# Optimization experiments

Measured on AMD Instinct MI355X. Metric: run time of the kernel, lower is better.

The kernel has to match this reference:

```python
import jax, jax.numpy as jnp
import numpy as np

B = 4; C_IN = 4; H = 32; W = 32; L = H * W
D_MODEL = 768; DEPTH = 4; D_INNER = 1536; D_STATE = 16; DT_RANK = 48; D_CONV = 4; FREQ = 256


def _zigzag_orders():
    idx = np.arange(L).reshape(H, W)
    z = idx.copy(); z[1::2] = z[1::2, ::-1]; row = z.reshape(-1)
    zt = idx.T.copy(); zt[1::2] = zt[1::2, ::-1]; col = zt.reshape(-1)
    base = [row, row[::-1].copy(), col, col[::-1].copy()]
    return np.stack([base[i % 4] for i in range(DEPTH)]).astype(np.int32)


def _sincos_pos_embed():
    def emb1d(dim, pos):
        omega = 1.0 / 10000 ** (np.arange(dim // 2, dtype=np.float64) / (dim / 2.0))
        out = np.einsum('m,d->md', pos.reshape(-1), omega)
        return np.concatenate([np.sin(out), np.cos(out)], axis=1)
    grid = np.stack(np.meshgrid(np.arange(W, dtype=np.float32), np.arange(H, dtype=np.float32)), 0)
    emb = np.concatenate([emb1d(D_MODEL // 2, grid[0]), emb1d(D_MODEL // 2, grid[1])], axis=1)
    return jnp.asarray(emb[None].astype(np.float32))  # [1, L, D]


def setup_inputs() -> dict:
    key = jax.random.key(0)
    ks = iter(jax.random.split(key, 24))
    def nrm(shape, s=0.02):
        return jax.random.normal(next(ks), shape, jnp.float32) * s
    inp = {}
    inp['x'] = jax.random.normal(next(ks), (B, C_IN, H, W), jnp.float32)
    inp['t'] = jax.random.uniform(next(ks), (B,), jnp.float32) * 1000.0
    inp['patch_w'] = nrm((D_MODEL, C_IN))
    inp['patch_b'] = jnp.zeros((D_MODEL,), jnp.float32)
    inp['pos_embed'] = _sincos_pos_embed()
    inp['t_w1'] = nrm((D_MODEL, FREQ))
    inp['t_b1'] = jnp.zeros((D_MODEL,), jnp.float32)
    inp['t_w2'] = nrm((D_MODEL, D_MODEL))
    inp['t_b2'] = jnp.zeros((D_MODEL,), jnp.float32)
    inp['norm_w'] = jnp.ones((DEPTH, D_MODEL), jnp.float32)
    inp['norm_b'] = jnp.zeros((DEPTH, D_MODEL), jnp.float32)
    inp['in_proj_w'] = nrm((DEPTH, 2 * D_INNER, D_MODEL))
    inp['conv_w'] = nrm((DEPTH, D_INNER, 1, D_CONV), 0.1)
    inp['conv_b'] = jnp.zeros((DEPTH, D_INNER), jnp.float32)
    inp['x_proj_w'] = nrm((DEPTH, DT_RANK + 2 * D_STATE, D_INNER))
    inp['dt_w'] = nrm((DEPTH, D_INNER, DT_RANK))
    inp['dt_b'] = jnp.full((DEPTH, D_INNER), -4.6, jnp.float32)  # softplus ~ 0.01
    inp['A_log'] = jnp.tile(jnp.log(jnp.arange(1, D_STATE + 1, dtype=jnp.float32)), (DEPTH, D_INNER, 1))
    inp['Dp'] = jnp.ones((DEPTH, D_INNER), jnp.float32)
    inp['out_proj_w'] = nrm((DEPTH, D_MODEL, D_INNER))
    inp['final_ada_w'] = nrm((2 * D_MODEL, D_MODEL))
    inp['final_ada_b'] = jnp.zeros((2 * D_MODEL,), jnp.float32)
    inp['final_lin_w'] = nrm((C_IN, D_MODEL))
    inp['final_lin_b'] = jnp.zeros((C_IN,), jnp.float32)
    inp['orders'] = jnp.asarray(_zigzag_orders())
    return inp


def _ln(v, w, b, eps=1e-5):
    m = v.mean(-1, keepdims=True)
    var = v.var(-1, keepdims=True)
    return (v - m) * jax.lax.rsqrt(var + eps) * w + b


def _forward(x, t, patch_w, patch_b, pos_embed, t_w1, t_b1, t_w2, t_b2, norm_w, norm_b,
             in_proj_w, conv_w, conv_b, x_proj_w, dt_w, dt_b, A_log, Dp, out_proj_w,
             final_ada_w, final_ada_b, final_lin_w, final_lin_b, orders):
    silu = jax.nn.silu
    # patch embed (patch_size=1): [B,C,H,W] -> [B,L,D]
    tok = x.reshape(B, C_IN, L).transpose(0, 2, 1)
    h = tok @ patch_w.T + patch_b + pos_embed
    # timestep embedding -> conditioning c
    half = FREQ // 2
    freqs = jnp.exp(-jnp.log(10000.0) * jnp.arange(half, dtype=jnp.float32) / half)
    ang = t[:, None] * freqs[None]
    temb = jnp.concatenate([jnp.cos(ang), jnp.sin(ang)], -1)
    c = silu(temb @ t_w1.T + t_b1) @ t_w2.T + t_b2

    for i in range(DEPTH):
        order = orders[i]
        inv = jnp.argsort(order)
        ho = h[:, order]                                   # zigzag permute tokens
        u = _ln(ho, norm_w[i], norm_b[i])
        # Mamba mixer
        xz = u @ in_proj_w[i].T                            # [B,L,2*di]
        xm, z = jnp.split(xz, 2, -1)
        xc = jax.lax.conv_general_dilated(
            xm.transpose(0, 2, 1), conv_w[i], (1,), [(D_CONV - 1, 0)],
            feature_group_count=D_INNER, dimension_numbers=('NCH', 'OIH', 'NCH'))
        xm = silu((xc + conv_b[i][None, :, None]).transpose(0, 2, 1))  # [B,L,di]
        dbl = xm @ x_proj_w[i].T
        dt = dbl[..., :DT_RANK]
        Bm = dbl[..., DT_RANK:DT_RANK + D_STATE]
        Cm = dbl[..., DT_RANK + D_STATE:]
        dt = jax.nn.softplus(dt @ dt_w[i].T + dt_b[i])     # [B,L,di]
        A = -jnp.exp(A_log[i])                             # [di,ds]
        def step(hs, inp):
            dt_t, B_t, C_t, x_t = inp                      # [B,di],[B,ds],[B,ds],[B,di]
            hs = jnp.exp(dt_t[..., None] * A) * hs + (dt_t * x_t)[..., None] * B_t[:, None, :]
            return hs, jnp.einsum('bds,bs->bd', hs, C_t)
        xs = (dt.transpose(1, 0, 2), Bm.transpose(1, 0, 2), Cm.transpose(1, 0, 2), xm.transpose(1, 0, 2))
        h0 = jnp.zeros((B, D_INNER, D_STATE), xm.dtype)
        _, ys = jax.lax.scan(step, h0, xs)
        y = ys.transpose(1, 0, 2) + Dp[i] * xm
        y = y * silu(z)
        ho = ho + y @ out_proj_w[i].T                      # residual
        h = ho[:, inv]                                     # undo zigzag permute

    # final layer: adaLN modulation + linear + unpatchify (p=1)
    shift, scale = jnp.split(silu(c) @ final_ada_w.T + final_ada_b, 2, -1)
    m = h.mean(-1, keepdims=True)
    v = h.var(-1, keepdims=True)
    hn = (h - m) * jax.lax.rsqrt(v + 1e-6)
    hn = hn * (1 + scale[:, None, :]) + shift[:, None, :]
    out = hn @ final_lin_w.T + final_lin_b                 # [B,L,C]
    return out.transpose(0, 2, 1).reshape(B, C_IN, H, W)


def reference(x, t, patch_w, patch_b, pos_embed, t_w1, t_b1, t_w2, t_b2, norm_w, norm_b,
              in_proj_w, conv_w, conv_b, x_proj_w, dt_w, dt_b, A_log, Dp, out_proj_w,
              final_ada_w, final_ada_b, final_lin_w, final_lin_b, orders):
    return _forward(x, t, patch_w, patch_b, pos_embed, t_w1, t_b1, t_w2, t_b2, norm_w, norm_b,
                    in_proj_w, conv_w, conv_b, x_proj_w, dt_w, dt_b, A_log, Dp, out_proj_w,
                    final_ada_w, final_ada_b, final_lin_w, final_lin_b, orders)
```

## Files before the change

kernel.cpp:

```cpp
#include <hip/hip_runtime.h>
#include <hip/hip_bf16.h>
#include <cstddef>

#define DEPTH_N 4
#define BATCH 4
#define LSEQ 1024
#define DM 768
#define DI 1536
#define DSN 16
#define TOK (BATCH*LSEQ)
#define LDSW 72
#define NCH 16
#define CL  (LSEQ/NCH)
#define SPLITO 3
#define NW1 (3072*DM)

typedef __hip_bfloat16 bf16_t;
typedef __bf16 bf16x8v __attribute__((ext_vector_type(8)));
typedef float f32x4v __attribute__((ext_vector_type(4)));
typedef float f32x2v __attribute__((ext_vector_type(2)));

__device__ __forceinline__ float bf2f(bf16_t v){ return __bfloat162float(v); }
__device__ __forceinline__ bf16_t f2bf(float v){ return __float2bfloat16(v); }
__device__ __forceinline__ float siluf(float x){ return x / (1.f + __expf(-x)); }

__device__ __forceinline__ float ldf(const void* p, size_t i, int f32){
  return f32 ? ((const float*)p)[i] : bf2f(((const bf16_t*)p)[i]);
}

__global__ void detect_kernel(const void* norm_w, int* flag){
  if (threadIdx.x==0 && blockIdx.x==0){
    const unsigned u = *(const unsigned*)norm_w;
    flag[0] = ((u & 0xFFFFu) == 0u) ? 1 : 0;
  }
}

__global__ __launch_bounds__(256) void inv_kernel(const int* __restrict__ orders, int* __restrict__ invb){
  const int idx = blockIdx.x*256 + threadIdx.x;
  const int i = idx >> 10;
  invb[i*LSEQ + orders[idx]] = idx & 1023;
}

__global__ __launch_bounds__(256) void cvtw_kernel(
    const void* __restrict__ ipw, size_t ipOff,
    const void* __restrict__ opw, size_t opOff,
    const int* __restrict__ flagp, bf16_t* __restrict__ wbuf)
{
  const int fl = flagp[0];
  size_t i = ((size_t)blockIdx.x*256 + threadIdx.x)*8;
  #pragma unroll
  for (int k=0;k<8;++k,++i){
    if (i < (size_t)NW1) wbuf[i] = f2bf(ldf(ipw, ipOff + i, fl));
    else                 wbuf[i] = f2bf(ldf(opw, opOff + (i - NW1), fl));
  }
}

template<int EPI>
__global__ __launch_bounds__(256,2) void gemm_bt(
    const bf16_t* __restrict__ A, int lda,
    const bf16_t* __restrict__ W, int ldw,
    int kChunk, const int* __restrict__ flagp,
    void* __restrict__ out0, void* __restrict__ out1,
    int ldOut, int nValid,
    const void* __restrict__ bias, size_t biasOff)
{
  __shared__ __align__(16) bf16_t As[128*LDSW];
  __shared__ __align__(16) bf16_t Ws[128*LDSW];
  const int fl   = flagp[0];
  const int tid  = threadIdx.x;
  const int m0   = blockIdx.x * 128;
  const int n0   = blockIdx.y * 128;
  const int kBase= blockIdx.z * kChunk;
  const int kIters = kChunk >> 6;
  const int lane = tid & 63;
  const int wv   = tid >> 6;
  const int wm   = wv & 1, wn = wv >> 1;
  const int srow = tid >> 3;
  const int scol = (tid & 7) << 3;
  const int mr   = lane & 15;
  const int kq   = (lane >> 4) << 3;

  f32x4v acc[4][4] = {};
  bf16x8v ra[4], rw[4];

  auto loadTile = [&](int kt){
    const int kk = kBase + (kt << 6);
    const bf16_t* ga = A + (size_t)(m0 + srow) * lda + kk + scol;
    const bf16_t* gw = W + (size_t)(n0 + srow) * ldw + kk + scol;
    #pragma unroll
    for (int g=0; g<4; ++g){
      ra[g] = *(const bf16x8v*)(ga + (size_t)(g*32)*lda);
      rw[g] = *(const bf16x8v*)(gw + (size_t)(g*32)*ldw);
    }
  };

  loadTile(0);
  for (int kt = 0; kt < kIters; ++kt) {
    __syncthreads();
    #pragma unroll
    for (int g=0; g<4; ++g){
      *(bf16x8v*)(As + (srow + 32*g)*LDSW + scol) = ra[g];
      *(bf16x8v*)(Ws + (srow + 32*g)*LDSW + scol) = rw[g];
    }
    __syncthreads();
    if (kt + 1 < kIters) loadTile(kt + 1);

    #pragma unroll
    for (int kk2=0; kk2<2; ++kk2){
      bf16x8v af[4], wfr[4];
      #pragma unroll
      for (int mt=0; mt<4; ++mt)
        af[mt] = *(const bf16x8v*)(As + (wm*64 + mt*16 + mr)*LDSW + kk2*32 + kq);
      #pragma unroll
      for (int nt=0; nt<4; ++nt)
        wfr[nt] = *(const bf16x8v*)(Ws + (wn*64 + nt*16 + mr)*LDSW + kk2*32 + kq);
      #pragma unroll
      for (int mt=0; mt<4; ++mt)
        #pragma unroll
        for (int nt=0; nt<4; ++nt)
          acc[mt][nt] = __builtin_amdgcn_mfma_f32_16x16x32_bf16(af[mt], wfr[nt], acc[mt][nt], 0, 0, 0);
    }
  }

  const int rq = (lane >> 4) << 2;
  const int nc = lane & 15;
  #pragma unroll
  for (int mt=0; mt<4; ++mt){
    #pragma unroll
    for (int nt=0; nt<4; ++nt){
      #pragma unroll
      for (int r=0; r<4; ++r){
        const int m = m0 + wm*64 + mt*16 + rq + r;
        const int n = n0 + wn*64 + nt*16 + nc;
        const float v = acc[mt][nt][r];
        if constexpr (EPI == 0) {
          ((float*)out0)[(size_t)blockIdx.z*TOK*DM + (size_t)m*ldOut + n] = v;
        } else if constexpr (EPI == 1) {
          if (n < nValid) atomicAdd((float*)out0 + (size_t)m*ldOut + n, v);
        } else if constexpr (EPI == 2) {
          const float xb = v + ldf(bias, biasOff + n, fl);
          const float sp = (xb > 20.f) ? xb : __logf(1.f + __expf(xb));
          ((bf16_t*)out0)[(size_t)m*ldOut + n] = f2bf(sp);
        } else {
          if (n < DI) ((bf16_t*)out0)[(size_t)m*DI + n]        = f2bf(v);
          else        ((bf16_t*)out1)[(size_t)m*DI + (n - DI)] = f2bf(v);
        }
      }
    }
  }
}

__global__ __launch_bounds__(256) void embed_kernel(
    const void* __restrict__ x, const void* __restrict__ pw,
    const void* __restrict__ pb, const void* __restrict__ pos,
    const int* __restrict__ flagp, float* __restrict__ h)
{
  const int fl = flagp[0];
  const int t = blockIdx.x; const int b = t >> 10, l = t & 1023;
  const float xc0 = ldf(x, (b*4+0)*1024 + l, fl);
  const float xc1 = ldf(x, (b*4+1)*1024 + l, fl);
  const float xc2 = ldf(x, (b*4+2)*1024 + l, fl);
  const float xc3 = ldf(x, (b*4+3)*1024 + l, fl);
  for (int d = threadIdx.x; d < DM; d += 256){
    float a = ldf(pb, d, fl) + ldf(pos, (size_t)l*DM + d, fl);
    a += xc0*ldf(pw, d*4+0, fl) + xc1*ldf(pw, d*4+1, fl)
       + xc2*ldf(pw, d*4+2, fl) + xc3*ldf(pw, d*4+3, fl);
    h[(size_t)t*DM + d] = a;
  }
}

__global__ __launch_bounds__(256) void temb1_kernel(
    const void* __restrict__ tin, const void* __restrict__ w1, const void* __restrict__ b1,
    const int* __restrict__ flagp, float* __restrict__ hid)
{
  const int fl = flagp[0];
  const int gid = blockIdx.x*4 + (threadIdx.x >> 6);
  const int lane = threadIdx.x & 63;
  const int b = gid / DM, d = gid % DM;
  const float tv = ldf(tin, b, fl);
  float a = 0.f;
  #pragma unroll
  for (int i = 0; i < 4; ++i){
    const int k = lane + i*64;
    const int kk = k & 127;
    const float fr = __expf(-logf(10000.f) * (float)kk / 128.f);
    const float ang = tv * fr;
    const float te = (k < 128) ? __cosf(ang) : __sinf(ang);
    a += te * ldf(w1, (size_t)d*256 + k, fl);
  }
  #pragma unroll
  for (int off=32; off>0; off>>=1) a += __shfl_down(a, off, 64);
  if (lane == 0) hid[b*DM + d] = siluf(a + ldf(b1, d, fl));
}

__global__ __launch_bounds__(256) void temb2_kernel(
    const float* __restrict__ hid, const void* __restrict__ w2, const void* __restrict__ b2,
    const int* __restrict__ flagp, float* __restrict__ cbuf)
{
  const int fl = flagp[0];
  const int gid = blockIdx.x*4 + (threadIdx.x >> 6);
  const int lane = threadIdx.x & 63;
  const int b = gid / DM, d = gid % DM;
  float a = 0.f;
  #pragma unroll
  for (int i = 0; i < 12; ++i){
    const int k = lane + i*64;
    a += hid[b*DM + k] * ldf(w2, (size_t)d*768 + k, fl);
  }
  #pragma unroll
  for (int off=32; off>0; off>>=1) a += __shfl_down(a, off, 64);
  if (lane == 0) cbuf[b*DM + d] = a + ldf(b2, d, fl);
}

__global__ __launch_bounds__(256) void ada_kernel(
    const float* __restrict__ cbuf, const void* __restrict__ aw,
    const void* __restrict__ ab, const int* __restrict__ flagp,
    float* __restrict__ scbuf)
{
  const int fl = flagp[0];
  const int gid = blockIdx.x*4 + (threadIdx.x >> 6);
  const int lane = threadIdx.x & 63;
  const int b = gid / 1536, n = gid % 1536;
  float a = 0.f;
  #pragma unroll
  for (int i = 0; i < 12; ++i){
    const int k = lane + i*64;
    a += siluf(cbuf[b*DM + k]) * ldf(aw, (size_t)n*768 + k, fl);
  }
  #pragma unroll
  for (int off=32; off>0; off>>=1) a += __shfl_down(a, off, 64);
  if (lane == 0) scbuf[b*1536 + n] = a + ldf(ab, n, fl);
}

__global__ __launch_bounds__(256) void ln_gather_kernel(
    float* __restrict__ h, const int* __restrict__ order,
    const int* __restrict__ invp, const float* __restrict__ yo,
    const void* __restrict__ nw, const void* __restrict__ nb, size_t nOff,
    const int* __restrict__ flagp, bf16_t* __restrict__ u)
{
  const int fl = flagp[0];
  const int t = blockIdx.x; const int b = t >> 10, j = t & 1023;
  const int tid = threadIdx.x;
  const int l = order[j];
  float* row = h + ((size_t)(b<<10) + l)*DM;
  float s=0.f, ss=0.f; float vbuf[3];
  if (invp){
    const float* yrow = yo + ((size_t)(b<<10) + invp[l])*DM;
    #pragma unroll
    for (int i2=0;i2<3;++i2){
      const int d = tid + i2*256;
      const float v = row[d] + yrow[d] + yrow[(size_t)TOK*DM + d] + yrow[(size_t)2*TOK*DM + d];
      row[d] = v;
      vbuf[i2]=v; s+=v; ss+=v*v;
    }
  } else {
    #pragma unroll
    for (int i2=0;i2<3;++i2){ const float v = row[tid + i2*256]; vbuf[i2]=v; s+=v; ss+=v*v; }
  }
  for (int off=32; off>0; off>>=1){ s += __shfl_down(s, off, 64); ss += __shfl_down(ss, off, 64); }
  __shared__ float r1[4], r2[4];
  if ((tid&63)==0){ r1[tid>>6]=s; r2[tid>>6]=ss; }
  __syncthreads();
  const float S  = r1[0]+r1[1]+r1[2]+r1[3];
  const float SS = r2[0]+r2[1]+r2[2]+r2[3];
  const float mean = S * (1.f/768.f);
  const float var  = fmaxf(SS * (1.f/768.f) - mean*mean, 0.f);
  const float rstd = rsqrtf(var + 1e-5f);
  #pragma unroll
  for (int i2=0;i2<3;++i2){
    const int d = tid + i2*256;
    const float v = (vbuf[i2]-mean)*rstd*ldf(nw, nOff+d, fl) + ldf(nb, nOff+d, fl);
    u[(size_t)t*DM + d] = f2bf(v);
  }
}

__global__ __launch_bounds__(256) void conv_kernel(
    const bf16_t* __restrict__ xm, const void* __restrict__ cw, size_t cwOff,
    const void* __restrict__ cb, size_t cbOff, const int* __restrict__ flagp,
    bf16_t* __restrict__ xcb)
{
  const int fl = flagp[0];
  const int idx = blockIdx.x*256 + threadIdx.x;
  const int d = idx % DI;
  const int t = idx / DI;
  const int b = t >> 10, j = t & 1023;
  float acc = ldf(cb, cbOff + d, fl);
  #pragma unroll
  for (int k=0;k<4;++k){
    const int jj = j - 3 + k;
    if (jj >= 0) acc += bf2f(xm[((size_t)(b<<10)+jj)*DI + d]) * ldf(cw, cwOff + d*4+k, fl);
  }
  xcb[idx] = f2bf(siluf(acc));
}

__global__ __launch_bounds__(256) void padw_kernel(
    const void* __restrict__ xpw, const void* __restrict__ dtw,
    const int* __restrict__ flagp,
    bf16_t* __restrict__ xw_pad, bf16_t* __restrict__ dtw_pad)
{
  const int fl = flagp[0];
  int idx = blockIdx.x*256 + threadIdx.x;
  const int NX = DEPTH_N*128*DI;
  const int ND = DEPTH_N*DI*64;
  if (idx < NX){
    const int i = idx / (128*DI); const int rem = idx % (128*DI);
    const int r = rem / DI; const int k = rem % DI;
    xw_pad[idx] = (r < 80) ? f2bf(ldf(xpw, ((size_t)i*80 + r)*DI + k, fl)) : f2bf(0.f);
  }
  idx -= NX;
  if (idx >= 0 && idx < ND){
    const int i = idx / (DI*64); const int rem = idx % (DI*64);
    const int n = rem / 64; const int k = rem % 64;
    dtw_pad[idx] = (k < 48) ? f2bf(ldf(dtw, ((size_t)i*DI + n)*48 + k, fl)) : f2bf(0.f);
  }
}

__global__ __launch_bounds__(256) void dta_kernel(const float* __restrict__ dbl, bf16_t* __restrict__ dtA)
{
  const int idx = blockIdx.x*256 + threadIdx.x;
  const int t = idx >> 6, k = idx & 63;
  dtA[idx] = (k < 48) ? f2bf(dbl[(size_t)t*80 + k]) : f2bf(0.f);
}

__global__ __launch_bounds__(256) void aprep_kernel(
    const void* __restrict__ alog, const int* __restrict__ flagp, float* __restrict__ Asb)
{
  const int fl = flagp[0];
  const int idx = blockIdx.x*256 + threadIdx.x;
  Asb[idx] = -__expf(ldf(alog, idx, fl));
}

__global__ __launch_bounds__(256) void scan1_kernel(
    const bf16_t* __restrict__ dtf, const bf16_t* __restrict__ xcb,
    const float* __restrict__ dbl, const float* __restrict__ Asl,
    float* __restrict__ Pb, float* __restrict__ Sb)
{
  const int tid = threadIdx.x;
  const int half = tid & 1, dl = tid >> 1;
  const int d0 = blockIdx.x*128, d = d0 + dl;
  const int b = blockIdx.y, c = blockIdx.z;
  const int so = half*8;
  __shared__ __align__(16) bf16_t sdt[16][128];
  __shared__ __align__(16) bf16_t sx[16][128];
  __shared__ __align__(16) float  sB[16][16];
  float As[8], S[8];
  *(f32x4v*)(As)   = *(const f32x4v*)(Asl + (size_t)d*16 + so);
  *(f32x4v*)(As+4) = *(const f32x4v*)(Asl + (size_t)d*16 + so + 4);
  #pragma unroll
  for (int s=0;s<8;++s) S[s]=0.f;
  float sumdt = 0.f;
  const int t0 = c*CL;
  const int qr = tid >> 4, cb2 = (tid & 15) << 3;
  const int jb = tid & 15;
  bf16x8v p_dt, p_x; float p_B;
  auto stage_load = [&](int p){
    const size_t tb = (size_t)(b<<10) + t0 + p*16 + qr;
    p_dt = *(const bf16x8v*)(dtf + tb*DI + d0 + cb2);
    p_x  = *(const bf16x8v*)(xcb + tb*DI + d0 + cb2);
    p_B  = dbl[tb*80 + 48 + jb];
  };
  stage_load(0);
  for (int p = 0; p < 4; ++p){
    __syncthreads();
    *(bf16x8v*)&sdt[qr][cb2] = p_dt;
    *(bf16x8v*)&sx[qr][cb2]  = p_x;
    sB[qr][jb] = p_B;
    __syncthreads();
    if (p+1 < 4) stage_load(p+1);
    for (int q = 0; q < 16; ++q){
      const float dt = bf2f(sdt[q][dl]);
      const float xv = bf2f(sx[q][dl]);
      const float dx = dt*xv;
      sumdt += dt;
      const f32x4v B0 = *(const f32x4v*)&sB[q][so];
      const f32x4v B1 = *(const f32x4v*)&sB[q][so+4];
      #pragma unroll
      for (int s=0;s<8;++s){
        const float a = __expf(dt*As[s]);
        S[s] = a*S[s] + dx*((s<4) ? B0[s] : B1[s-4]);
      }
    }
  }
  float* po = Pb + (size_t)(b*NCH + c)*DI*16 + (size_t)d*16 + so;
  float* sp = Sb + (size_t)(b*NCH + c)*DI*16 + (size_t)d*16 + so;
  f32x4v pv0, pv1, sv0, sv1;
  #pragma unroll
  for (int k2=0;k2<4;++k2){
    pv0[k2]=__expf(As[k2]*sumdt); pv1[k2]=__expf(As[4+k2]*sumdt);
    sv0[k2]=S[k2]; sv1[k2]=S[4+k2];
  }
  *(f32x4v*)(po)   = pv0; *(f32x4v*)(po+4) = pv1;
  *(f32x4v*)(sp)   = sv0; *(f32x4v*)(sp+4) = sv1;
}

__global__ __launch_bounds__(256) void scan2_kernel(
    const float* __restrict__ Pb, const float* __restrict__ Sb,
    float* __restrict__ Hin)
{
  const int idx = blockIdx.x*256 + threadIdx.x;
  const int b = idx / (DI*16), r = idx % (DI*16);
  float hi = 0.f;
  for (int c = 0; c < NCH; ++c){
    const size_t o = (size_t)(b*NCH + c)*DI*16 + r;
    const float p = Pb[o], s = Sb[o];
    Hin[o] = hi;
    hi = p*hi + s;
  }
}

__global__ __launch_bounds__(256) void scan3_kernel(
    const bf16_t* __restrict__ dtf, const bf16_t* __restrict__ xcb,
    const float* __restrict__ dbl, const bf16_t* __restrict__ zb,
    const float* __restrict__ Asl,
    const void* __restrict__ dpw, size_t dOff, const int* __restrict__ flagp,
    const float* __restrict__ Hin, bf16_t* __restrict__ y2)
{
  const int fl = flagp[0];
  const int tid = threadIdx.x;
  const int half = tid & 1, dl = tid >> 1;
  const int d0 = blockIdx.x*128, d = d0 + dl;
  const int b = blockIdx.y, c = blockIdx.z;
  const int so = half*8;
  __shared__ __align__(16) bf16_t sdt[16][128];
  __shared__ __align__(16) bf16_t sx[16][128];
  __shared__ __align__(16) bf16_t sz[16][128];
  __shared__ __align__(16) float  sBC[16][32];
  float As[8], hs[8];
  *(f32x4v*)(As)   = *(const f32x4v*)(Asl + (size_t)d*16 + so);
  *(f32x4v*)(As+4) = *(const f32x4v*)(Asl + (size_t)d*16 + so + 4);
  const float* hp = Hin + (size_t)(b*NCH + c)*DI*16 + (size_t)d*16 + so;
  *(f32x4v*)(hs)   = *(const f32x4v*)(hp);
  *(f32x4v*)(hs+4) = *(const f32x4v*)(hp+4);
  const float Dv = ldf(dpw, dOff + d, fl);
  const int t0 = c*CL;
  const int qr = tid >> 4, cb2 = (tid & 15) << 3;
  const int jc = (tid & 15) * 2;
  bf16x8v p_dt, p_x, p_z; f32x2v p_bc;
  auto stage_load = [&](int p){
    const size_t tb = (size_t)(b<<10) + t0 + p*16 + qr;
    p_dt = *(const bf16x8v*)(dtf + tb*DI + d0 + cb2);
    p_x  = *(const bf16x8v*)(xcb + tb*DI + d0 + cb2);
    p_z  = *(const bf16x8v*)(zb  + tb*DI + d0 + cb2);
    p_bc = *(const f32x2v*)(dbl + tb*80 + 48 + jc);
  };
  stage_load(0);
  for (int p = 0; p < 4; ++p){
    __syncthreads();
    *(bf16x8v*)&sdt[qr][cb2] = p_dt;
    *(bf16x8v*)&sx[qr][cb2]  = p_x;
    *(bf16x8v*)&sz[qr][cb2]  = p_z;
    sBC[qr][jc] = p_bc[0]; sBC[qr][jc+1] = p_bc[1];
    __syncthreads();
    if (p+1 < 4) stage_load(p+1);
    for (int q = 0; q < 16; ++q){
      const float dt = bf2f(sdt[q][dl]);
      const float xv = bf2f(sx[q][dl]);
      const float zv = bf2f(sz[q][dl]);
      const float dx = dt*xv;
      const f32x4v B0 = *(const f32x4v*)&sBC[q][so];
      const f32x4v B1 = *(const f32x4v*)&sBC[q][so+4];
      const f32x4v C0 = *(const f32x4v*)&sBC[q][16+so];
      const f32x4v C1 = *(const f32x4v*)&sBC[q][16+so+4];
      float ya=0.f, yb=0.f;
      #pragma unroll
      for (int s=0;s<8;++s){
        const float a = __expf(dt*As[s]);
        hs[s] = a*hs[s] + dx*((s<4) ? B0[s] : B1[s-4]);
        const float pr = hs[s]*((s<4) ? C0[s] : C1[s-4]);
        if (s<4) ya += pr; else yb += pr;
      }
      float term = ya + yb;
      term += __shfl_xor(term, 1, 64);
      if (half == 0){
        float y = term + Dv*xv;
        y *= siluf(zv);
        y2[((size_t)(b<<10) + t0 + p*16 + q)*DI + d] = f2bf(y);
      }
    }
  }
}

__global__ __launch_bounds__(256) void final_kernel(
    const float* __restrict__ h, const int* __restrict__ invp,
    const float* __restrict__ yo, const float* __restrict__ scbuf,
    const void* __restrict__ lw, const void* __restrict__ lb,
    const int* __restrict__ flagp, void* __restrict__ outp)
{
  const int fl = flagp[0];
  const int t = blockIdx.x; const int b = t >> 10, l = t & 1023;
  const int tid = threadIdx.x;
  const float* row = h + (size_t)t*DM;
  const float* yrow = yo + ((size_t)(b<<10) + invp[l])*DM;
  float s=0.f, ss=0.f; float vbuf[3];
  #pragma unroll
  for (int i2=0;i2<3;++i2){
    const int d = tid + i2*256;
    const float v = row[d] + yrow[d] + yrow[(size_t)TOK*DM + d] + yrow[(size_t)2*TOK*DM + d];
    vbuf[i2]=v; s+=v; ss+=v*v;
  }
  for (int off=32; off>0; off>>=1){ s += __shfl_down(s,off,64); ss += __shfl_down(ss,off,64); }
  __shared__ float r1[4], r2[4];
  if ((tid&63)==0){ r1[tid>>6]=s; r2[tid>>6]=ss; }
  __syncthreads();
  const float S=r1[0]+r1[1]+r1[2]+r1[3], SS=r2[0]+r2[1]+r2[2]+r2[3];
  const float mean = S*(1.f/768.f);
  const float var  = fmaxf(SS*(1.f/768.f) - mean*mean, 0.f);
  const float rstd = rsqrtf(var + 1e-6f);
  float a0=0.f,a1=0.f,a2=0.f,a3=0.f;
  #pragma unroll
  for (int i2=0;i2<3;++i2){
    const int d = tid + i2*256;
    float hn = (vbuf[i2]-mean)*rstd;
    hn = hn*(1.f + scbuf[b*1536 + 768 + d]) + scbuf[b*1536 + d];
    a0 += hn*ldf(lw, 0*768+d, fl);
    a1 += hn*ldf(lw, 1*768+d, fl);
    a2 += hn*ldf(lw, 2*768+d, fl);
    a3 += hn*ldf(lw, 3*768+d, fl);
  }
  for (int off=32; off>0; off>>=1){
    a0 += __shfl_down(a0,off,64); a1 += __shfl_down(a1,off,64);
    a2 += __shfl_down(a2,off,64); a3 += __shfl_down(a3,off,64);
  }
  __shared__ float rc[4][4];
  if ((tid&63)==0){ const int w=tid>>6; rc[w][0]=a0; rc[w][1]=a1; rc[w][2]=a2; rc[w][3]=a3; }
  __syncthreads();
  if (tid==0){
    #pragma unroll
    for (int c=0;c<4;++c){
      const float vv = rc[0][c]+rc[1][c]+rc[2][c]+rc[3][c] + ldf(lb, c, fl);
      const size_t oi = (size_t)b*4096 + c*1024 + l;
      if (fl) ((float*)outp)[oi] = vv;
      else    ((bf16_t*)outp)[oi] = f2bf(vv);
    }
  }
}

extern "C" void kernel_launch(void* const* d_in, const int* in_sizes, int n_in,
                              void* d_out, int out_size, void* d_ws, size_t ws_size,
                              hipStream_t stream)
{
  const void* x        = d_in[0];
  const void* tin      = d_in[1];
  const void* patch_w  = d_in[2];
  const void* patch_b  = d_in[3];
  const void* pos      = d_in[4];
  const void* t_w1     = d_in[5];
  const void* t_b1     = d_in[6];
  const void* t_w2     = d_in[7];
  const void* t_b2     = d_in[8];
  const void* norm_w   = d_in[9];
  const void* norm_b   = d_in[10];
  const void* in_proj_w= d_in[11];
  const void* conv_w   = d_in[12];
  const void* conv_b   = d_in[13];
  const void* x_proj_w = d_in[14];
  const void* dt_w     = d_in[15];
  const void* dt_b     = d_in[16];
  const void* A_log    = d_in[17];
  const void* Dp       = d_in[18];
  const void* out_proj_w=d_in[19];
  const void* ada_w    = d_in[20];
  const void* ada_b    = d_in[21];
  const void* lin_w    = d_in[22];
  const void* lin_b    = d_in[23];
  const int*  orders   = (const int*)d_in[24];
  (void)in_sizes; (void)n_in; (void)out_size; (void)ws_size;

  char* w = (char*)d_ws;
  auto alloc = [&](size_t bytes)->char*{ char* p = w; w += (bytes + 255) & ~(size_t)255; return p; };
  int*    flag   = (int*)   alloc(256);
  int*    invb   = (int*)   alloc((size_t)DEPTH_N*LSEQ*4);
  float*  h      = (float*) alloc((size_t)TOK*DM*4);
  float*  hid    = (float*) alloc((size_t)4*768*4);
  float*  cbuf   = (float*) alloc((size_t)4*768*4);
  float*  scbuf  = (float*) alloc((size_t)4*1536*4);
  bf16_t* u      = (bf16_t*)alloc((size_t)TOK*DM*2);
  bf16_t* xmb    = (bf16_t*)alloc((size_t)TOK*DI*2);
  bf16_t* zb     = (bf16_t*)alloc((size_t)TOK*DI*2);
  bf16_t* xcb    = (bf16_t*)alloc((size_t)TOK*DI*2);
  float*  dbl    = (float*) alloc((size_t)TOK*80*4);
  bf16_t* dtA    = (bf16_t*)alloc((size_t)TOK*64*2);
  bf16_t* y2     = (bf16_t*)alloc((size_t)TOK*DI*2);
  bf16_t* xw_pad = (bf16_t*)alloc((size_t)DEPTH_N*128*DI*2);
  bf16_t* dtw_pad= (bf16_t*)alloc((size_t)DEPTH_N*DI*64*2);
  float*  Asb    = (float*) alloc((size_t)DEPTH_N*DI*16*4);
  float*  Pb     = (float*) alloc((size_t)BATCH*NCH*DI*16*4);
  float*  Sb     = (float*) alloc((size_t)BATCH*NCH*DI*16*4);
  bf16_t* wbuf   = (bf16_t*)alloc((size_t)(NW1 + DM*DI)*2);
  bf16_t* dtf    = xmb;
  float*  Hin    = (float*)u;
  float*  yo     = (float*)xmb;

  detect_kernel<<<1,64,0,stream>>>(norm_w, flag);
  inv_kernel<<<(DEPTH_N*LSEQ)/256,256,0,stream>>>(orders, invb);
  embed_kernel<<<TOK,256,0,stream>>>(x, patch_w, patch_b, pos, flag, h);
  temb1_kernel<<<(BATCH*DM)/4,256,0,stream>>>(tin, t_w1, t_b1, flag, hid);
  temb2_kernel<<<(BATCH*DM)/4,256,0,stream>>>(hid, t_w2, t_b2, flag, cbuf);
  ada_kernel<<<(BATCH*1536)/4,256,0,stream>>>(cbuf, ada_w, ada_b, flag, scbuf);
  padw_kernel<<<(DEPTH_N*128*DI + DEPTH_N*DI*64)/256,256,0,stream>>>(x_proj_w, dt_w, flag, xw_pad, dtw_pad);
  aprep_kernel<<<(DEPTH_N*DI*16)/256,256,0,stream>>>(A_log, flag, Asb);

  for (int i = 0; i < DEPTH_N; ++i){
    const int* order_i = orders + i*LSEQ;
    const int* invPrev = (i > 0) ? (invb + (i-1)*LSEQ) : nullptr;
    cvtw_kernel<<<(NW1 + DM*DI)/(256*8),256,0,stream>>>(
        in_proj_w, (size_t)i*NW1, out_proj_w, (size_t)i*DM*DI, flag, wbuf);
    ln_gather_kernel<<<TOK,256,0,stream>>>(h, order_i, invPrev, yo,
        norm_w, norm_b, (size_t)i*DM, flag, u);
    gemm_bt<4><<<dim3(32,24,1),256,0,stream>>>(u, DM,
        wbuf, DM, 768, flag,
        xmb, zb, DI, 3072, nullptr, 0);
    conv_kernel<<<(TOK*DI)/256,256,0,stream>>>(xmb, conv_w, (size_t)i*DI*4, conv_b, (size_t)i*DI, flag, xcb);
    hipMemsetAsync(dbl, 0, (size_t)TOK*80*4, stream);
    gemm_bt<1><<<dim3(32,1,4),256,0,stream>>>(xcb, DI,
        xw_pad + (size_t)i*128*DI, DI, 384, flag,
        dbl, nullptr, 80, 80, nullptr, 0);
    dta_kernel<<<(TOK*64)/256,256,0,stream>>>(dbl, dtA);
    gemm_bt<2><<<dim3(32,12,1),256,0,stream>>>(dtA, 64,
        dtw_pad + (size_t)i*DI*64, 64, 64, flag,
        dtf, nullptr, DI, DI, dt_b, (size_t)i*DI);
    scan1_kernel<<<dim3(DI/128,BATCH,NCH),256,0,stream>>>(dtf, xcb, dbl,
        Asb + (size_t)i*DI*16, Pb, Sb);
    scan2_kernel<<<(BATCH*DI*16)/256,256,0,stream>>>(Pb, Sb, Hin);
    scan3_kernel<<<dim3(DI/128,BATCH,NCH),256,0,stream>>>(dtf, xcb, dbl, zb,
        Asb + (size_t)i*DI*16, Dp, (size_t)i*DI, flag, Hin, y2);
    gemm_bt<0><<<dim3(32,6,SPLITO),256,0,stream>>>(y2, DI,
        wbuf + NW1, DI, DI/SPLITO, flag,
        yo, nullptr, DM, DM, nullptr, 0);
  }
  final_kernel<<<TOK,256,0,stream>>>(h, invb + 3*LSEQ, yo, scbuf, lin_w, lin_b, flag, d_out);
}
```

Before: 966.9 us.

## Use direct global-to-LDS loads with XOR swizzle in GEMM; batch weight conversion

The GEMM tile loader now uses global_load_lds to write 16-byte chunks straight into an unpadded, XOR-swizzled shared-memory layout instead of staging through registers into a padded layout. The old register prefetch of the next tile is dropped, so each k-step now waits for its own loads. Weight conversion for all four layers is done in one launch before the layer loop into a larger buffer, which removes three launches and their serialization. This uses more scratch memory, and the GEMM loses its load/compute overlap.

```diff
diff --git a/kernel.cpp b/kernel.cpp
--- a/kernel.cpp
+++ b/kernel.cpp
@@ -9,11 +9,11 @@
 #define DI 1536
 #define DSN 16
 #define TOK (BATCH*LSEQ)
-#define LDSW 72
 #define NCH 16
 #define CL  (LSEQ/NCH)
 #define SPLITO 3
 #define NW1 (3072*DM)
+#define NWL (NW1 + DM*DI)
 
 typedef __hip_bfloat16 bf16_t;
 typedef __bf16 bf16x8v __attribute__((ext_vector_type(8)));
@@ -28,6 +28,12 @@
   return f32 ? ((const float*)p)[i] : bf2f(((const bf16_t*)p)[i]);
 }
 
+__device__ __forceinline__ void gld16(const bf16_t* g, bf16_t* l){
+  __builtin_amdgcn_global_load_lds(
+      (const __attribute__((address_space(1))) void*)g,
+      (__attribute__((address_space(3))) void*)l, 16, 0, 0);
+}
+
 __global__ void detect_kernel(const void* norm_w, int* flag){
   if (threadIdx.x==0 && blockIdx.x==0){
     const unsigned u = *(const unsigned*)norm_w;
@@ -42,16 +48,19 @@
 }
 
 __global__ __launch_bounds__(256) void cvtw_kernel(
-    const void* __restrict__ ipw, size_t ipOff,
-    const void* __restrict__ opw, size_t opOff,
+    const void* __restrict__ ipw, const void* __restrict__ opw,
     const int* __restrict__ flagp, bf16_t* __restrict__ wbuf)
 {
   const int fl = flagp[0];
-  size_t i = ((size_t)blockIdx.x*256 + threadIdx.x)*8;
-  #pragma unroll
-  for (int k=0;k<8;++k,++i){
-    if (i < (size_t)NW1) wbuf[i] = f2bf(ldf(ipw, ipOff + i, fl));
-    else                 wbuf[i] = f2bf(ldf(opw, opOff + (i - NW1), fl));
+  const int i = blockIdx.y;
+  size_t j = ((size_t)blockIdx.x*256 + threadIdx.x)*8;
+  bf16_t* wb = wbuf + (size_t)i*NWL;
+  const size_t ipOff = (size_t)i*NW1;
+  const size_t opOff = (size_t)i*(size_t)DM*DI;
+  #pragma unroll
+  for (int k=0;k<8;++k,++j){
+    if (j < (size_t)NW1) wb[j] = f2bf(ldf(ipw, ipOff + j, fl));
+    else                 wb[j] = f2bf(ldf(opw, opOff + (j - NW1), fl));
   }
 }
 
@@ -64,8 +73,8 @@
     int ldOut, int nValid,
     const void* __restrict__ bias, size_t biasOff)
 {
-  __shared__ __align__(16) bf16_t As[128*LDSW];
-  __shared__ __align__(16) bf16_t Ws[128*LDSW];
+  __shared__ __align__(16) bf16_t As[128*64];
+  __shared__ __align__(16) bf16_t Ws[128*64];
   const int fl   = flagp[0];
   const int tid  = threadIdx.x;
   const int m0   = blockIdx.x * 128;
@@ -76,44 +85,36 @@
   const int wv   = tid >> 6;
   const int wm   = wv & 1, wn = wv >> 1;
   const int srow = tid >> 3;
-  const int scol = (tid & 7) << 3;
+  const int scol = ((tid & 7) ^ (srow & 7)) << 3;
+  const int ldst = tid << 3;
   const int mr   = lane & 15;
   const int kq   = (lane >> 4) << 3;
+  const int xr   = (mr & 7) << 3;
 
   f32x4v acc[4][4] = {};
-  bf16x8v ra[4], rw[4];
-
-  auto loadTile = [&](int kt){
+
+  for (int kt = 0; kt < kIters; ++kt) {
     const int kk = kBase + (kt << 6);
+    __syncthreads();
     const bf16_t* ga = A + (size_t)(m0 + srow) * lda + kk + scol;
     const bf16_t* gw = W + (size_t)(n0 + srow) * ldw + kk + scol;
     #pragma unroll
     for (int g=0; g<4; ++g){
-      ra[g] = *(const bf16x8v*)(ga + (size_t)(g*32)*lda);
-      rw[g] = *(const bf16x8v*)(gw + (size_t)(g*32)*ldw);
-    }
-  };
-
-  loadTile(0);
-  for (int kt = 0; kt < kIters; ++kt) {
-    __syncthreads();
-    #pragma unroll
-    for (int g=0; g<4; ++g){
-      *(bf16x8v*)(As + (srow + 32*g)*LDSW + scol) = ra[g];
-      *(bf16x8v*)(Ws + (srow + 32*g)*LDSW + scol) = rw[g];
+      gld16(ga + (size_t)(g*32)*lda, As + g*2048 + ldst);
+      gld16(gw + (size_t)(g*32)*ldw, Ws + g*2048 + ldst);
     }
     __syncthreads();
-    if (kt + 1 < kIters) loadTile(kt + 1);
 
     #pragma unroll
     for (int kk2=0; kk2<2; ++kk2){
       bf16x8v af[4], wfr[4];
+      const int co = (kk2*32 + kq) ^ xr;
       #pragma unroll
       for (int mt=0; mt<4; ++mt)
-        af[mt] = *(const bf16x8v*)(As + (wm*64 + mt*16 + mr)*LDSW + kk2*32 + kq);
+        af[mt] = *(const bf16x8v*)(As + (wm*64 + mt*16 + mr)*64 + co);
       #pragma unroll
       for (int nt=0; nt<4; ++nt)
-        wfr[nt] = *(const bf16x8v*)(Ws + (wn*64 + nt*16 + mr)*LDSW + kk2*32 + kq);
+        wfr[nt] = *(const bf16x8v*)(Ws + (wn*64 + nt*16 + mr)*64 + co);
       #pragma unroll
       for (int mt=0; mt<4; ++mt)
         #pragma unroll
@@ -586,7 +587,7 @@
   float*  Asb    = (float*) alloc((size_t)DEPTH_N*DI*16*4);
   float*  Pb     = (float*) alloc((size_t)BATCH*NCH*DI*16*4);
   float*  Sb     = (float*) alloc((size_t)BATCH*NCH*DI*16*4);
-  bf16_t* wbuf   = (bf16_t*)alloc((size_t)(NW1 + DM*DI)*2);
+  bf16_t* wbuf   = (bf16_t*)alloc((size_t)DEPTH_N*NWL*2);
   bf16_t* dtf    = xmb;
   float*  Hin    = (float*)u;
   float*  yo     = (float*)xmb;
@@ -599,16 +600,17 @@
   ada_kernel<<<(BATCH*1536)/4,256,0,stream>>>(cbuf, ada_w, ada_b, flag, scbuf);
   padw_kernel<<<(DEPTH_N*128*DI + DEPTH_N*DI*64)/256,256,0,stream>>>(x_proj_w, dt_w, flag, xw_pad, dtw_pad);
   aprep_kernel<<<(DEPTH_N*DI*16)/256,256,0,stream>>>(A_log, flag, Asb);
+  cvtw_kernel<<<dim3(NWL/(256*8),DEPTH_N),256,0,stream>>>(in_proj_w, out_proj_w, flag, wbuf);
 
   for (int i = 0; i < DEPTH_N; ++i){
     const int* order_i = orders + i*LSEQ;
     const int* invPrev = (i > 0) ? (invb + (i-1)*LSEQ) : nullptr;
-    cvtw_kernel<<<(NW1 + DM*DI)/(256*8),256,0,stream>>>(
-        in_proj_w, (size_t)i*NW1, out_proj_w, (size_t)i*DM*DI, flag, wbuf);
+    const bf16_t* wIn  = wbuf + (size_t)i*NWL;
+    const bf16_t* wOut = wbuf + (size_t)i*NWL + NW1;
     ln_gather_kernel<<<TOK,256,0,stream>>>(h, order_i, invPrev, yo,
         norm_w, norm_b, (size_t)i*DM, flag, u);
     gemm_bt<4><<<dim3(32,24,1),256,0,stream>>>(u, DM,
-        wbuf, DM, 768, flag,
+        wIn, DM, 768, flag,
         xmb, zb, DI, 3072, nullptr, 0);
     conv_kernel<<<(TOK*DI)/256,256,0,stream>>>(xmb, conv_w, (size_t)i*DI*4, conv_b, (size_t)i*DI, flag, xcb);
     hipMemsetAsync(dbl, 0, (size_t)TOK*80*4, stream);
@@ -625,7 +627,7 @@
     scan3_kernel<<<dim3(DI/128,BATCH,NCH),256,0,stream>>>(dtf, xcb, dbl, zb,
         Asb + (size_t)i*DI*16, Dp, (size_t)i*DI, flag, Hin, y2);
     gemm_bt<0><<<dim3(32,6,SPLITO),256,0,stream>>>(y2, DI,
-        wbuf + NW1, DI, DI/SPLITO, flag,
+        wOut, DI, DI/SPLITO, flag,
         yo, nullptr, DM, DM, nullptr, 0);
   }
   final_kernel<<<TOK,256,0,stream>>>(h, invb + 3*LSEQ, yo, scbuf, lin_w, lin_b, flag, d_out);
```

Measured after the change: 951.1 us. Within noise of the previous version (-1.6%).
